# Optimization experiments

Measured on AMD Instinct MI355X. Metric: run time of the kernel, lower is better.

## Reference

```python
import jax, jax.numpy as jnp
import numpy as np

LEAK = 0.95
EPS = 1e-4
THRESH = 1.0


def spike_fn(x):
    # forward of SurrogateBPFunction: heaviside(x > 0)
    return (x > 0).astype(x.dtype)


def setup_inputs() -> dict:
    key = jax.random.key(0)
    k1, k2, k3 = jax.random.split(key, 3)
    T, B, D_in, H, C = 20, 512, 4096, 1024, 100
    z = jax.random.normal(k1, (T, B, D_in), dtype=jnp.float32)
    # xavier_uniform with gain=2: bound = 2 * sqrt(6/(fan_in+fan_out))
    b1 = 2.0 * np.sqrt(6.0 / (D_in + H))
    W1 = jax.random.uniform(k2, (H, D_in), dtype=jnp.float32, minval=-b1, maxval=b1)
    b2 = 2.0 * np.sqrt(6.0 / (H + C))
    W2 = jax.random.uniform(k3, (C, H), dtype=jnp.float32, minval=-b2, maxval=b2)
    bn_gamma = jnp.ones((T, H), dtype=jnp.float32)
    return {"z": z, "W1": W1, "bn_gamma": bn_gamma, "W2": W2}


def reference(z, W1, bn_gamma, W2):
    T = z.shape[0]
    B = z.shape[1]
    H = W1.shape[0]
    C = W2.shape[0]

    def step(carry, xs):
        mem1, mem2 = carry
        inp_t, gamma = xs  # inp_t: [B, D_in], gamma: [H]
        h = jnp.einsum('bd,hd->bh', inp_t, W1)  # fc1, no bias
        # BatchNorm1d (training-mode batch stats, affine weight, no bias)
        mean = h.mean(axis=0)
        var = h.var(axis=0)  # biased variance, matches torch BN
        h = gamma * (h - mean) * jax.lax.rsqrt(var + EPS)
        mem1 = LEAK * mem1 + h
        mem_thr = mem1 / THRESH - 1.0
        out = spike_fn(mem_thr)
        rst = jnp.where(mem_thr > 0, THRESH, 0.0).astype(mem1.dtype)
        mem1 = mem1 - rst
        mem2 = mem2 + jnp.einsum('bh,ch->bc', out, W2)
        return (mem1, mem2), None

    mem1_0 = jnp.zeros((B, H), dtype=z.dtype)
    mem2_0 = jnp.zeros((B, C), dtype=z.dtype)
    (mem1, mem2), _ = jax.lax.scan(step, (mem1_0, mem2_0), (z, bn_gamma))
    return mem2 / T
```

## Files before the change

kernel.cpp:

```cpp
#include <hip/hip_runtime.h>
#include <hip/hip_bf16.h>
#include <stdint.h>

typedef _Float16 half8 __attribute__((ext_vector_type(8)));
typedef _Float16 half4v __attribute__((ext_vector_type(4)));
typedef float f32x4 __attribute__((ext_vector_type(4)));

#define T_STEPS 20
#define B_SZ 512
#define D_IN 4096
#define H_SZ 1024
#define C_SZ 100
#define M_TOT (T_STEPS * B_SZ)
#define BK 32

__device__ __forceinline__ void gload16(const _Float16* g, _Float16* l) {
  __builtin_amdgcn_global_load_lds(
      (const __attribute__((address_space(1))) void*)g,
      (__attribute__((address_space(3))) void*)l, 16, 0, 0);
}

__global__ void k_split4(const float* __restrict__ x, _Float16* __restrict__ hi,
                         _Float16* __restrict__ lo) {
  int64_t i = (int64_t)blockIdx.x * blockDim.x + threadIdx.x;
  float4 v = ((const float4* __restrict__)x)[i];
  half4v h, l;
  h.x = (_Float16)v.x; l.x = (_Float16)(v.x - (float)h.x);
  h.y = (_Float16)v.y; l.y = (_Float16)(v.y - (float)h.y);
  h.z = (_Float16)v.z; l.z = (_Float16)(v.z - (float)h.z);
  h.w = (_Float16)v.w; l.w = (_Float16)(v.w - (float)h.w);
  ((half4v*)hi)[i] = h;
  ((half4v*)lo)[i] = l;
}

__global__ void k_prep_w2(const float* __restrict__ w2, _Float16* __restrict__ hi,
                          _Float16* __restrict__ lo) {
  int i = blockIdx.x * 256 + threadIdx.x;
  float v = (i < C_SZ * H_SZ) ? w2[i] : 0.0f;
  _Float16 h = (_Float16)v;
  hi[i] = h;
  lo[i] = (_Float16)(v - (float)h);
}

__global__ __launch_bounds__(256) void k_gemm1(
    const _Float16* __restrict__ Ahi, const _Float16* __restrict__ Alo,
    const _Float16* __restrict__ Whi, const _Float16* __restrict__ Wlo,
    float* __restrict__ Hbuf) {
  __shared__ _Float16 sAh[128 * BK];
  __shared__ _Float16 sAl[128 * BK];
  __shared__ _Float16 sWh[128 * BK];
  __shared__ _Float16 sWl[128 * BK];

  const int tid = threadIdx.x;
  const int bid = blockIdx.x;
  const int xcd = bid & 7;
  const int q = bid >> 3;
  const int mt = xcd * 10 + (q >> 3);
  const int nt = q & 7;
  const int64_t m0 = (int64_t)mt * 128;
  const int64_t n0 = (int64_t)nt * 128;

  const int srow = tid >> 2;
  const int scol = (tid & 3) * 8;
  const _Float16* gAh = Ahi + (m0 + srow) * D_IN + scol;
  const _Float16* gAl = Alo + (m0 + srow) * D_IN + scol;
  const _Float16* gWh = Whi + (n0 + srow) * D_IN + scol;
  const _Float16* gWl = Wlo + (n0 + srow) * D_IN + scol;
  const int ls = tid * 8;
  const int64_t g2 = (int64_t)64 * D_IN;

  const int lane = tid & 63;
  const int wid = tid >> 6;
  const int wm = (wid >> 1) * 64;
  const int wn = (wid & 1) * 64;
  const int fr = lane & 15;
  const int quad = lane >> 4;

  f32x4 acc[4][4] = {};

  for (int kt = 0; kt < D_IN; kt += BK) {
    __syncthreads();
    gload16(gAh + kt, &sAh[ls]);
    gload16(gAh + kt + g2, &sAh[ls + 2048]);
    gload16(gAl + kt, &sAl[ls]);
    gload16(gAl + kt + g2, &sAl[ls + 2048]);
    gload16(gWh + kt, &sWh[ls]);
    gload16(gWh + kt + g2, &sWh[ls + 2048]);
    gload16(gWl + kt, &sWl[ls]);
    gload16(gWl + kt + g2, &sWl[ls + 2048]);
    __syncthreads();

    half8 ah[4], al[4], bh[4], bl[4];
#pragma unroll
    for (int i = 0; i < 4; ++i) {
      const int ro = (wm + i * 16 + fr) * BK + quad * 8;
      ah[i] = *(const half8*)&sAh[ro];
      al[i] = *(const half8*)&sAl[ro];
    }
#pragma unroll
    for (int j = 0; j < 4; ++j) {
      const int ro = (wn + j * 16 + fr) * BK + quad * 8;
      bh[j] = *(const half8*)&sWh[ro];
      bl[j] = *(const half8*)&sWl[ro];
    }
#pragma unroll
    for (int i = 0; i < 4; ++i) {
#pragma unroll
      for (int j = 0; j < 4; ++j) {
        acc[i][j] = __builtin_amdgcn_mfma_f32_16x16x32_f16(ah[i], bh[j], acc[i][j], 0, 0, 0);
        acc[i][j] = __builtin_amdgcn_mfma_f32_16x16x32_f16(ah[i], bl[j], acc[i][j], 0, 0, 0);
        acc[i][j] = __builtin_amdgcn_mfma_f32_16x16x32_f16(al[i], bh[j], acc[i][j], 0, 0, 0);
      }
    }
  }

#pragma unroll
  for (int i = 0; i < 4; ++i) {
#pragma unroll
    for (int r = 0; r < 4; ++r) {
      const int64_t row = m0 + wm + i * 16 + quad * 4 + r;
      float* dst = Hbuf + row * H_SZ + n0 + wn + fr;
#pragma unroll
      for (int j = 0; j < 4; ++j) dst[j * 16] = acc[i][j][r];
    }
  }
}

__global__ void k_stats(const float* __restrict__ Hbuf, const float* __restrict__ gamma,
                        float* __restrict__ scale, float* __restrict__ shift) {
  const int t = blockIdx.y;
  const int n = blockIdx.x * 256 + threadIdx.x;
  const float* p = Hbuf + (int64_t)t * B_SZ * H_SZ + n;
  float s = 0.f, s2 = 0.f;
  for (int b = 0; b < B_SZ; ++b) {
    float v = p[(int64_t)b * H_SZ];
    s += v;
    s2 += v * v;
  }
  const float mean = s * (1.0f / B_SZ);
  const float var = s2 * (1.0f / B_SZ) - mean * mean;
  const float rs = rsqrtf(var + 1e-4f);
  const float sc = gamma[t * H_SZ + n] * rs;
  scale[t * H_SZ + n] = sc;
  shift[t * H_SZ + n] = -mean * sc;
}

__global__ void k_recur(const float* __restrict__ Hbuf, const float* __restrict__ scale,
                        const float* __restrict__ shift, _Float16* __restrict__ S) {
  const int idx = blockIdx.x * 256 + threadIdx.x;
  const int b = idx >> 10;
  const int h = idx & 1023;
  float mem = 0.f;
  int cnt = 0;
#pragma unroll
  for (int t = 0; t < T_STEPS; ++t) {
    float v = Hbuf[((int64_t)(t * B_SZ + b) << 10) + h];
    v = v * scale[(t << 10) + h] + shift[(t << 10) + h];
    mem = 0.95f * mem + v;
    if (mem - 1.0f > 0.0f) {
      ++cnt;
      mem -= 1.0f;
    }
  }
  S[idx] = (_Float16)cnt;
}

__global__ void k_gemm2(const _Float16* __restrict__ S, const _Float16* __restrict__ W2h,
                        const _Float16* __restrict__ W2l, float* __restrict__ out) {
  const int wid = threadIdx.x >> 6;
  const int lane = threadIdx.x & 63;
  const int m0 = blockIdx.y * 64 + wid * 16;
  const int n0 = blockIdx.x * 16;
  const int fr = lane & 15;
  const int quad = lane >> 4;

  const _Float16* sp = S + (int64_t)(m0 + fr) * H_SZ + quad * 8;
  const _Float16* wph = W2h + (int64_t)(n0 + fr) * H_SZ + quad * 8;
  const _Float16* wpl = W2l + (int64_t)(n0 + fr) * H_SZ + quad * 8;

  f32x4 acc = {0.f, 0.f, 0.f, 0.f};
#pragma unroll 4
  for (int k = 0; k < H_SZ; k += 32) {
    half8 a = *(const half8*)(sp + k);
    half8 bh = *(const half8*)(wph + k);
    half8 bl = *(const half8*)(wpl + k);
    acc = __builtin_amdgcn_mfma_f32_16x16x32_f16(a, bh, acc, 0, 0, 0);
    acc = __builtin_amdgcn_mfma_f32_16x16x32_f16(a, bl, acc, 0, 0, 0);
  }
  const int col = n0 + fr;
  if (col < C_SZ) {
#pragma unroll
    for (int r = 0; r < 4; ++r) {
      const int row = m0 + quad * 4 + r;
      out[row * C_SZ + col] = acc[r] * (1.0f / T_STEPS);
    }
  }
}

extern "C" void kernel_launch(void* const* d_in, const int* in_sizes, int n_in,
                              void* d_out, int out_size, void* d_ws, size_t ws_size,
                              hipStream_t stream) {
  const float* z = (const float*)d_in[0];
  const float* W1 = (const float*)d_in[1];
  const float* gamma = (const float*)d_in[2];
  const float* W2 = (const float*)d_in[3];
  float* out = (float*)d_out;

  char* ws = (char*)d_ws;
  size_t off = 0;
  auto alloc = [&](size_t bytes) -> void* {
    void* p = ws + off;
    off += (bytes + 255) & ~(size_t)255;
    return p;
  };
  _Float16* Ahi = (_Float16*)alloc((size_t)M_TOT * D_IN * 2);
  _Float16* Alo = (_Float16*)alloc((size_t)M_TOT * D_IN * 2);
  _Float16* Whi = (_Float16*)alloc((size_t)H_SZ * D_IN * 2);
  _Float16* Wlo = (_Float16*)alloc((size_t)H_SZ * D_IN * 2);
  float* Hbuf = (float*)alloc((size_t)M_TOT * H_SZ * 4);
  float* scale = (float*)alloc((size_t)T_STEPS * H_SZ * 4);
  float* shift = (float*)alloc((size_t)T_STEPS * H_SZ * 4);
  _Float16* S = (_Float16*)alloc((size_t)B_SZ * H_SZ * 2);
  _Float16* W2h = (_Float16*)alloc((size_t)112 * H_SZ * 2);
  _Float16* W2l = (_Float16*)alloc((size_t)112 * H_SZ * 2);

  k_split4<<<(M_TOT * (int64_t)D_IN) / 1024, 256, 0, stream>>>(z, Ahi, Alo);
  k_split4<<<(H_SZ * D_IN) / 1024, 256, 0, stream>>>(W1, Whi, Wlo);
  k_prep_w2<<<(112 * H_SZ) / 256, 256, 0, stream>>>(W2, W2h, W2l);

  k_gemm1<<<640, 256, 0, stream>>>(Ahi, Alo, Whi, Wlo, Hbuf);

  dim3 gs(H_SZ / 256, T_STEPS);
  k_stats<<<gs, 256, 0, stream>>>(Hbuf, gamma, scale, shift);

  k_recur<<<(B_SZ * H_SZ) / 256, 256, 0, stream>>>(Hbuf, scale, shift, S);

  dim3 g2(7, 8);
  k_gemm2<<<g2, 256, 0, stream>>>(S, W2h, W2l, out);
}
```

Measured before the change: 577.3 us.

## Fuse fp32-to-fp16 hi/lo split of z into GEMM1 and parallelize BN stats

Removes the separate split kernel over z and its two fp16 workspace copies. GEMM1 now loads fp32 z straight into registers, splits it into hi/lo halves with round-toward-zero packed conversions, and writes them to LDS in an MFMA-fragment-friendly layout, prefetching the next K tile during compute. The BN statistics kernel now splits the batch reduction across 16 thread rows with a shared-memory combine, so it launches more blocks. The trade-off is extra VALU conversion work inside the GEMM main loop and RTZ rounding of the hi part instead of round-to-nearest.

```diff
diff --git a/kernel.cpp b/kernel.cpp
--- a/kernel.cpp
+++ b/kernel.cpp
@@ -18,6 +18,27 @@
   __builtin_amdgcn_global_load_lds(
       (const __attribute__((address_space(1))) void*)g,
       (__attribute__((address_space(3))) void*)l, 16, 0, 0);
+}
+
+struct HL {
+  half8 h;
+  half8 l;
+};
+__device__ __forceinline__ HL split8(float4 a, float4 b) {
+  HL r;
+  auto p0 = __builtin_amdgcn_cvt_pkrtz(a.x, a.y);
+  auto p1 = __builtin_amdgcn_cvt_pkrtz(a.z, a.w);
+  auto p2 = __builtin_amdgcn_cvt_pkrtz(b.x, b.y);
+  auto p3 = __builtin_amdgcn_cvt_pkrtz(b.z, b.w);
+  r.h[0] = p0.x; r.h[1] = p0.y; r.h[2] = p1.x; r.h[3] = p1.y;
+  r.h[4] = p2.x; r.h[5] = p2.y; r.h[6] = p3.x; r.h[7] = p3.y;
+  auto q0 = __builtin_amdgcn_cvt_pkrtz(a.x - (float)p0.x, a.y - (float)p0.y);
+  auto q1 = __builtin_amdgcn_cvt_pkrtz(a.z - (float)p1.x, a.w - (float)p1.y);
+  auto q2 = __builtin_amdgcn_cvt_pkrtz(b.x - (float)p2.x, b.y - (float)p2.y);
+  auto q3 = __builtin_amdgcn_cvt_pkrtz(b.z - (float)p3.x, b.w - (float)p3.y);
+  r.l[0] = q0.x; r.l[1] = q0.y; r.l[2] = q1.x; r.l[3] = q1.y;
+  r.l[4] = q2.x; r.l[5] = q2.y; r.l[6] = q3.x; r.l[7] = q3.y;
+  return r;
 }
 
 __global__ void k_split4(const float* __restrict__ x, _Float16* __restrict__ hi,
@@ -43,15 +64,18 @@
 }
 
 __global__ __launch_bounds__(256) void k_gemm1(
-    const _Float16* __restrict__ Ahi, const _Float16* __restrict__ Alo,
+    const float* __restrict__ Z,
     const _Float16* __restrict__ Whi, const _Float16* __restrict__ Wlo,
     float* __restrict__ Hbuf) {
-  __shared__ _Float16 sAh[128 * BK];
-  __shared__ _Float16 sAl[128 * BK];
-  __shared__ _Float16 sWh[128 * BK];
-  __shared__ _Float16 sWl[128 * BK];
+  __shared__ _Float16 sAh[4096];
+  __shared__ _Float16 sAl[4096];
+  __shared__ _Float16 sWh[4096];
+  __shared__ _Float16 sWl[4096];
 
   const int tid = threadIdx.x;
+  const int lane = tid & 63;
+  const int w = tid >> 6;
+
   const int bid = blockIdx.x;
   const int xcd = bid & 7;
   const int q = bid >> 3;
@@ -60,48 +84,66 @@
   const int64_t m0 = (int64_t)mt * 128;
   const int64_t n0 = (int64_t)nt * 128;
 
-  const int srow = tid >> 2;
-  const int scol = (tid & 3) * 8;
-  const _Float16* gAh = Ahi + (m0 + srow) * D_IN + scol;
-  const _Float16* gAl = Alo + (m0 + srow) * D_IN + scol;
-  const _Float16* gWh = Whi + (n0 + srow) * D_IN + scol;
-  const _Float16* gWl = Wlo + (n0 + srow) * D_IN + scol;
-  const int ls = tid * 8;
-  const int64_t g2 = (int64_t)64 * D_IN;
-
-  const int lane = tid & 63;
-  const int wid = tid >> 6;
-  const int wm = (wid >> 1) * 64;
-  const int wn = (wid & 1) * 64;
+  const int sfr = tid & 15;
+  const int sq = (tid >> 4) & 3;
+  const float* gz = Z + (m0 + (int64_t)(w * 16 + sfr)) * D_IN + sq * 8;
+  const int aws = w * 512 + (sq * 16 + sfr) * 8;
+
+  const _Float16* gW = Whi + (n0 + (int64_t)(w * 16 + (lane & 15))) * D_IN + (lane >> 4) * 8;
+  const _Float16* gWl2 = Wlo + (n0 + (int64_t)(w * 16 + (lane & 15))) * D_IN + (lane >> 4) * 8;
+  const int wws = w * 512 + lane * 8;
+  const int64_t g2w = (int64_t)64 * D_IN;
+
+  const int wm = (w >> 1) * 64;
+  const int wn = (w & 1) * 64;
+  const int ra = (wm >> 4) * 512 + lane * 8;
+  const int rb = (wn >> 4) * 512 + lane * 8;
   const int fr = lane & 15;
   const int quad = lane >> 4;
 
   f32x4 acc[4][4] = {};
 
+  float4 r00 = *(const float4*)(gz);
+  float4 r01 = *(const float4*)(gz + 4);
+  float4 r10 = *(const float4*)(gz + g2w);
+  float4 r11 = *(const float4*)(gz + g2w + 4);
+
   for (int kt = 0; kt < D_IN; kt += BK) {
     __syncthreads();
-    gload16(gAh + kt, &sAh[ls]);
-    gload16(gAh + kt + g2, &sAh[ls + 2048]);
-    gload16(gAl + kt, &sAl[ls]);
-    gload16(gAl + kt + g2, &sAl[ls + 2048]);
-    gload16(gWh + kt, &sWh[ls]);
-    gload16(gWh + kt + g2, &sWh[ls + 2048]);
-    gload16(gWl + kt, &sWl[ls]);
-    gload16(gWl + kt + g2, &sWl[ls + 2048]);
+
+    gload16(gW + kt, &sWh[wws]);
+    gload16(gW + kt + g2w, &sWh[wws + 2048]);
+    gload16(gWl2 + kt, &sWl[wws]);
+    gload16(gWl2 + kt + g2w, &sWl[wws + 2048]);
+
+    {
+      HL p0 = split8(r00, r01);
+      *(half8*)&sAh[aws] = p0.h;
+      *(half8*)&sAl[aws] = p0.l;
+      HL p1 = split8(r10, r11);
+      *(half8*)&sAh[aws + 2048] = p1.h;
+      *(half8*)&sAl[aws + 2048] = p1.l;
+    }
+
     __syncthreads();
 
+    if (kt + BK < D_IN) {
+      r00 = *(const float4*)(gz + kt + BK);
+      r01 = *(const float4*)(gz + kt + BK + 4);
+      r10 = *(const float4*)(gz + kt + BK + g2w);
+      r11 = *(const float4*)(gz + kt + BK + g2w + 4);
+    }
+
     half8 ah[4], al[4], bh[4], bl[4];
 #pragma unroll
     for (int i = 0; i < 4; ++i) {
-      const int ro = (wm + i * 16 + fr) * BK + quad * 8;
-      ah[i] = *(const half8*)&sAh[ro];
-      al[i] = *(const half8*)&sAl[ro];
+      ah[i] = *(const half8*)&sAh[ra + i * 512];
+      al[i] = *(const half8*)&sAl[ra + i * 512];
     }
 #pragma unroll
     for (int j = 0; j < 4; ++j) {
-      const int ro = (wn + j * 16 + fr) * BK + quad * 8;
-      bh[j] = *(const half8*)&sWh[ro];
-      bl[j] = *(const half8*)&sWl[ro];
+      bh[j] = *(const half8*)&sWh[rb + j * 512];
+      bl[j] = *(const half8*)&sWl[rb + j * 512];
     }
 #pragma unroll
     for (int i = 0; i < 4; ++i) {
@@ -129,20 +171,36 @@
 __global__ void k_stats(const float* __restrict__ Hbuf, const float* __restrict__ gamma,
                         float* __restrict__ scale, float* __restrict__ shift) {
   const int t = blockIdx.y;
-  const int n = blockIdx.x * 256 + threadIdx.x;
-  const float* p = Hbuf + (int64_t)t * B_SZ * H_SZ + n;
+  const int tx = threadIdx.x & 15;
+  const int ty = threadIdx.x >> 4;
+  const int h = blockIdx.x * 16 + tx;
+  const float* p = Hbuf + ((int64_t)t * B_SZ + ty * 32) * H_SZ + h;
   float s = 0.f, s2 = 0.f;
-  for (int b = 0; b < B_SZ; ++b) {
-    float v = p[(int64_t)b * H_SZ];
+#pragma unroll 8
+  for (int i = 0; i < 32; ++i) {
+    float v = p[(int64_t)i * H_SZ];
     s += v;
     s2 += v * v;
   }
-  const float mean = s * (1.0f / B_SZ);
-  const float var = s2 * (1.0f / B_SZ) - mean * mean;
-  const float rs = rsqrtf(var + 1e-4f);
-  const float sc = gamma[t * H_SZ + n] * rs;
-  scale[t * H_SZ + n] = sc;
-  shift[t * H_SZ + n] = -mean * sc;
+  __shared__ float ss[16][16];
+  __shared__ float sq[16][16];
+  ss[ty][tx] = s;
+  sq[ty][tx] = s2;
+  __syncthreads();
+  if (ty == 0) {
+    float a = 0.f, b = 0.f;
+#pragma unroll
+    for (int k = 0; k < 16; ++k) {
+      a += ss[k][tx];
+      b += sq[k][tx];
+    }
+    const float mean = a * (1.0f / B_SZ);
+    const float var = b * (1.0f / B_SZ) - mean * mean;
+    const float rs = rsqrtf(var + 1e-4f);
+    const float sc = gamma[t * H_SZ + h] * rs;
+    scale[t * H_SZ + h] = sc;
+    shift[t * H_SZ + h] = -mean * sc;
+  }
 }
 
 __global__ void k_recur(const float* __restrict__ Hbuf, const float* __restrict__ scale,
@@ -213,8 +271,6 @@
     off += (bytes + 255) & ~(size_t)255;
     return p;
   };
-  _Float16* Ahi = (_Float16*)alloc((size_t)M_TOT * D_IN * 2);
-  _Float16* Alo = (_Float16*)alloc((size_t)M_TOT * D_IN * 2);
   _Float16* Whi = (_Float16*)alloc((size_t)H_SZ * D_IN * 2);
   _Float16* Wlo = (_Float16*)alloc((size_t)H_SZ * D_IN * 2);
   float* Hbuf = (float*)alloc((size_t)M_TOT * H_SZ * 4);
@@ -224,13 +280,12 @@
   _Float16* W2h = (_Float16*)alloc((size_t)112 * H_SZ * 2);
   _Float16* W2l = (_Float16*)alloc((size_t)112 * H_SZ * 2);
 
-  k_split4<<<(M_TOT * (int64_t)D_IN) / 1024, 256, 0, stream>>>(z, Ahi, Alo);
   k_split4<<<(H_SZ * D_IN) / 1024, 256, 0, stream>>>(W1, Whi, Wlo);
   k_prep_w2<<<(112 * H_SZ) / 256, 256, 0, stream>>>(W2, W2h, W2l);
 
-  k_gemm1<<<640, 256, 0, stream>>>(Ahi, Alo, Whi, Wlo, Hbuf);
-
-  dim3 gs(H_SZ / 256, T_STEPS);
+  k_gemm1<<<640, 256, 0, stream>>>(z, Whi, Wlo, Hbuf);
+
+  dim3 gs(H_SZ / 16, T_STEPS);
   k_stats<<<gs, 256, 0, stream>>>(Hbuf, gamma, scale, shift);
 
   k_recur<<<(B_SZ * H_SZ) / 256, 256, 0, stream>>>(Hbuf, scale, shift, S);
```

New measurement: 591.3 us. 2.4% more time.
